# Performance work log

Measured on AMD Instinct MI355X. Metric: run time of the kernel, lower is better.

The kernel has to match this reference:

```python
import jax, jax.numpy as jnp
import numpy as np


def setup_inputs() -> dict:
    key = jax.random.key(0)
    k1, k2 = jax.random.split(key)
    from_points = jax.random.normal(k1, (16384, 64), dtype=jnp.float32)
    to_points = jax.random.normal(k2, (16384, 64), dtype=jnp.float32)
    return {"from_points": from_points, "to_points": to_points}


def reference(from_points, to_points):
    # Squared L2 distance matrix [N, M] via ||a||^2 + ||b||^2 - 2 a.b,
    # avoiding the O(N*M*D) broadcasted intermediate of the original.
    a_sq = jnp.sum(from_points * from_points, axis=-1)          # [N]
    b_sq = jnp.sum(to_points * to_points, axis=-1)              # [M]
    cross = jnp.einsum('nd,md->nm', from_points, to_points)     # [N, M]
    dist_mat = a_sq[:, None] + b_sq[None, :] - 2.0 * cross      # [N, M]
    # Row-wise min (nearest neighbor squared distance), then sum.
    return jnp.sum(jnp.min(dist_mat, axis=1))
```

## Files before the change

kernel.cpp:

```cpp
#include <hip/hip_runtime.h>
#include <stdint.h>

#define N_PTS 16384
#define TSPLITS 32
#define TO_TILES 16
#define FGPB 16
#define NBLOCKS (TSPLITS * (256 / FGPB))

typedef __attribute__((ext_vector_type(4)))  int i32x4;
typedef __attribute__((ext_vector_type(16))) int i32x16;

__device__ __forceinline__ int imin(int a, int b) { return a < b ? a : b; }
__device__ __forceinline__ int itree16(i32x16 a) {
    int m0 = imin(imin(a[0],  a[1]),  a[2]);
    int m1 = imin(imin(a[3],  a[4]),  a[5]);
    int m2 = imin(imin(a[6],  a[7]),  a[8]);
    int m3 = imin(imin(a[9],  a[10]), a[11]);
    int m4 = imin(imin(a[12], a[13]), a[14]);
    int m5 = imin(imin(a[15], m0), m1);
    return imin(imin(imin(m2, m3), m4), m5);
}
__device__ __forceinline__ int q8(float x) {
    int q = __float2int_rn(x);
    return q < -127 ? -127 : (q > 127 ? 127 : q);
}

__global__ __launch_bounds__(256) void prep_kernel(
        const float* __restrict__ from_pts, const float* __restrict__ to_pts,
        float* __restrict__ a_sq, int* __restrict__ bsqi,
        char* __restrict__ BfQ, char* __restrict__ AtoQ,
        float* __restrict__ out) {
    int gid = blockIdx.x * 256 + threadIdx.x;
    int row = gid >> 3;
    int sub = gid & 7;
    bool isFrom = row < N_PTS;
    int r = row & (N_PTS - 1);
    const float* src = isFrom ? from_pts : to_pts;
    float4 v0 = ((const float4*)src)[r * 16 + sub * 2];
    float4 v1 = ((const float4*)src)[r * 16 + sub * 2 + 1];
    float s = v0.x*v0.x + v0.y*v0.y + v0.z*v0.z + v0.w*v0.w
            + v1.x*v1.x + v1.y*v1.y + v1.z*v1.z + v1.w*v1.w;
    s += __shfl_xor(s, 1); s += __shfl_xor(s, 2); s += __shfl_xor(s, 4);
    float sc = isFrom ? -16.0f : 16.0f;
    int q0 = q8(v0.x*sc), q1 = q8(v0.y*sc), q2 = q8(v0.z*sc), q3 = q8(v0.w*sc);
    int q4 = q8(v1.x*sc), q5 = q8(v1.y*sc), q6 = q8(v1.z*sc), q7 = q8(v1.w*sc);
    int2 w;
    w.x = (q0 & 255) | ((q1 & 255) << 8) | ((q2 & 255) << 16) | (q3 << 24);
    w.y = (q4 & 255) | ((q5 & 255) << 8) | ((q6 & 255) << 16) | (q7 << 24);
    int st = r >> 5;
    int m  = r & 31;
    int kb = sub >> 2, h = (sub >> 1) & 1, half8 = sub & 1;
    size_t off = (((size_t)st * 2 + kb) * 64 + h * 32 + m) * 16 + 8 * half8;
    if (isFrom) {
        *(int2*)(BfQ + off) = w;
        if (sub == 0) a_sq[r] = s;
    } else {
        *(int2*)(AtoQ + off) = w;
        if (sub == 0)
            bsqi[st * 32 + ((m >> 2) & 1) * 16 + (m & 3) + 4 * (m >> 3)] =
                __float2int_rn(128.0f * s);
    }
    if (gid == 0) out[0] = 0.0f;
}

__global__ __launch_bounds__(512, 4) void main_kernel(
        const char* __restrict__ BfQ, const char* __restrict__ AtoQ,
        const int* __restrict__ bsqi, int* __restrict__ pmin) {
    __shared__ __align__(16) char abuf[32768];

    const int tid = threadIdx.x;
    const int lane = tid & 63;
    const int l31 = lane & 31;
    const int h   = lane >> 5;
    const int wv  = tid >> 6;
    const int ts  = blockIdx.x >> 4;
    const int bg  = blockIdx.x & 15;
    const int gtb = ts * TO_TILES;

    #pragma unroll
    for (int j2 = 0; j2 < 4; j2++) {
        int j = wv * 4 + j2;
        const char* g = AtoQ +
            (((size_t)(gtb + (j >> 1)) * 2 + (j & 1)) * 64 + lane) * 16;
        char* l = &abuf[j * 1024];
        __builtin_amdgcn_global_load_lds(
            (const __attribute__((address_space(1))) unsigned int*)g,
            (__attribute__((address_space(3))) unsigned int*)l, 16, 0, 0);
    }
    __syncthreads();

    #pragma unroll 1
    for (int f2 = 0; f2 < 2; f2++) {
        const int fg = bg * FGPB + f2 * 8 + wv;
        i32x4 Bf0[2], Bf1[2];
        #pragma unroll
        for (int kb = 0; kb < 2; kb++) {
            Bf0[kb] = *(const i32x4*)(BfQ + (((size_t)(2 * fg)     * 2 + kb) * 64 + lane) * 16);
            Bf1[kb] = *(const i32x4*)(BfQ + (((size_t)(2 * fg + 1) * 2 + kb) * 64 + lane) * 16);
        }
        int rmin0 = 0x7FFFFFFF, rmin1 = 0x7FFFFFFF;

        #pragma unroll 1
        for (int t = 0; t < TO_TILES; t++) {
            i32x4 A0 = *(const i32x4*)&abuf[((t * 2 + 0) * 64 + lane) * 16];
            i32x4 A1 = *(const i32x4*)&abuf[((t * 2 + 1) * 64 + lane) * 16];
            union { int4 f[4]; i32x16 v; } cu;
            const int4* cp = (const int4*)(bsqi + (gtb + t) * 32 + h * 16);
            cu.f[0] = cp[0]; cu.f[1] = cp[1]; cu.f[2] = cp[2]; cu.f[3] = cp[3];

            i32x16 acc0 = __builtin_amdgcn_mfma_i32_32x32x32_i8(A0, Bf0[0], cu.v, 0, 0, 0);
            i32x16 acc1 = __builtin_amdgcn_mfma_i32_32x32x32_i8(A0, Bf1[0], cu.v, 0, 0, 0);
            acc0 = __builtin_amdgcn_mfma_i32_32x32x32_i8(A1, Bf0[1], acc0, 0, 0, 0);
            acc1 = __builtin_amdgcn_mfma_i32_32x32x32_i8(A1, Bf1[1], acc1, 0, 0, 0);
            rmin0 = imin(rmin0, itree16(acc0));
            rmin1 = imin(rmin1, itree16(acc1));
        }

        rmin0 = imin(rmin0, __shfl_xor(rmin0, 32));
        rmin1 = imin(rmin1, __shfl_xor(rmin1, 32));
        if (lane < 32) {
            pmin[(size_t)ts * N_PTS + fg * 64 + l31]      = rmin0;
            pmin[(size_t)ts * N_PTS + fg * 64 + 32 + l31] = rmin1;
        }
    }
}

__global__ __launch_bounds__(256) void finish_kernel(
        const float* __restrict__ a_sq, const int* __restrict__ pmin,
        float* __restrict__ out) {
    int r = blockIdx.x * 256 + threadIdx.x;
    int m = pmin[r];
    #pragma unroll
    for (int s = 1; s < TSPLITS; s++)
        m = imin(m, pmin[(size_t)s * N_PTS + r]);
    float v = a_sq[r] + (float)m * 0.0078125f;
    #pragma unroll
    for (int k = 1; k < 64; k <<= 1) v += __shfl_xor(v, k);
    __shared__ float red[4];
    if ((threadIdx.x & 63) == 0) red[threadIdx.x >> 6] = v;
    __syncthreads();
    if (threadIdx.x == 0)
        atomicAdd(out, red[0] + red[1] + red[2] + red[3]);
}

extern "C" void kernel_launch(void* const* d_in, const int* in_sizes, int n_in,
                              void* d_out, int out_size, void* d_ws, size_t ws_size,
                              hipStream_t stream) {
    const float* from_pts = (const float*)d_in[0];
    const float* to_pts   = (const float*)d_in[1];
    char* ws = (char*)d_ws;
    float* a_sq = (float*)ws;
    int*   bsqi = (int*)(ws + (64 << 10));
    int*   pmin = (int*)(ws + (128 << 10));
    char*  BfQ  = ws + (128 << 10) + (2 << 20);
    char*  AtoQ = ws + (128 << 10) + (3 << 20);

    prep_kernel<<<(2 * N_PTS * 8) / 256, 256, 0, stream>>>(
        from_pts, to_pts, a_sq, bsqi, BfQ, AtoQ, (float*)d_out);
    main_kernel<<<NBLOCKS, 512, 0, stream>>>(BfQ, AtoQ, bsqi, pmin);
    finish_kernel<<<N_PTS / 256, 256, 0, stream>>>(a_sq, pmin, (float*)d_out);
}
```

Before: 83.42 us.

## Switch int8 distance MFMA from 32x32x32 to 16x16x64 with 8 from-tiles per wave

Replaces the 32x32x32 int8 MFMA tiles with 16x16x64 tiles, which cover the full K=64 in one instruction. The quantized data layout in the prep kernel and the b_sq bias layout are reorganized to match. Each wave now keeps eight from-point tiles in registers and loops over 32 to-tiles from LDS, using 256-thread blocks instead of 512. The aim is to cut per-result min-reduction work (4 accumulator values instead of 16) and chained MFMA dependencies, and to raise reuse of each LDS A load across 8 MFMAs. The cost is higher register pressure from B[8] and rmin[8], plus a different occupancy and grid shape.

```diff
diff --git a/kernel.cpp b/kernel.cpp
--- a/kernel.cpp
+++ b/kernel.cpp
@@ -3,23 +3,12 @@
 
 #define N_PTS 16384
 #define TSPLITS 32
-#define TO_TILES 16
-#define FGPB 16
-#define NBLOCKS (TSPLITS * (256 / FGPB))
+#define ATILES 32
+#define NBLOCKS (TSPLITS * 32)
 
-typedef __attribute__((ext_vector_type(4)))  int i32x4;
-typedef __attribute__((ext_vector_type(16))) int i32x16;
+typedef __attribute__((ext_vector_type(4))) int i32x4;
 
 __device__ __forceinline__ int imin(int a, int b) { return a < b ? a : b; }
-__device__ __forceinline__ int itree16(i32x16 a) {
-    int m0 = imin(imin(a[0],  a[1]),  a[2]);
-    int m1 = imin(imin(a[3],  a[4]),  a[5]);
-    int m2 = imin(imin(a[6],  a[7]),  a[8]);
-    int m3 = imin(imin(a[9],  a[10]), a[11]);
-    int m4 = imin(imin(a[12], a[13]), a[14]);
-    int m5 = imin(imin(a[15], m0), m1);
-    return imin(imin(imin(m2, m3), m4), m5);
-}
 __device__ __forceinline__ int q8(float x) {
     int q = __float2int_rn(x);
     return q < -127 ? -127 : (q > 127 ? 127 : q);
@@ -47,41 +36,36 @@
     int2 w;
     w.x = (q0 & 255) | ((q1 & 255) << 8) | ((q2 & 255) << 16) | (q3 << 24);
     w.y = (q4 & 255) | ((q5 & 255) << 8) | ((q6 & 255) << 16) | (q7 << 24);
-    int st = r >> 5;
-    int m  = r & 31;
-    int kb = sub >> 2, h = (sub >> 1) & 1, half8 = sub & 1;
-    size_t off = (((size_t)st * 2 + kb) * 64 + h * 32 + m) * 16 + 8 * half8;
+    int st = r >> 4;
+    int m  = r & 15;
+    int qg = sub >> 1, halfj = sub & 1;
+    size_t off = (((size_t)st * 64) + qg * 16 + m) * 16 + 8 * halfj;
     if (isFrom) {
         *(int2*)(BfQ + off) = w;
         if (sub == 0) a_sq[r] = s;
     } else {
         *(int2*)(AtoQ + off) = w;
-        if (sub == 0)
-            bsqi[st * 32 + ((m >> 2) & 1) * 16 + (m & 3) + 4 * (m >> 3)] =
-                __float2int_rn(128.0f * s);
+        if (sub == 0) bsqi[r] = __float2int_rn(128.0f * s);
     }
     if (gid == 0) out[0] = 0.0f;
 }
 
-__global__ __launch_bounds__(512, 4) void main_kernel(
+__global__ __launch_bounds__(256, 5) void main_kernel(
         const char* __restrict__ BfQ, const char* __restrict__ AtoQ,
         const int* __restrict__ bsqi, int* __restrict__ pmin) {
     __shared__ __align__(16) char abuf[32768];
 
     const int tid = threadIdx.x;
     const int lane = tid & 63;
-    const int l31 = lane & 31;
-    const int h   = lane >> 5;
     const int wv  = tid >> 6;
-    const int ts  = blockIdx.x >> 4;
-    const int bg  = blockIdx.x & 15;
-    const int gtb = ts * TO_TILES;
+    const int ts  = blockIdx.x >> 5;
+    const int bg  = blockIdx.x & 31;
+    const int gst = ts * ATILES;
 
     #pragma unroll
-    for (int j2 = 0; j2 < 4; j2++) {
-        int j = wv * 4 + j2;
-        const char* g = AtoQ +
-            (((size_t)(gtb + (j >> 1)) * 2 + (j & 1)) * 64 + lane) * 16;
+    for (int j2 = 0; j2 < 8; j2++) {
+        int j = wv * 8 + j2;
+        const char* g = AtoQ + ((size_t)(gst + j) * 64 + lane) * 16;
         char* l = &abuf[j * 1024];
         __builtin_amdgcn_global_load_lds(
             (const __attribute__((address_space(1))) unsigned int*)g,
@@ -89,39 +73,39 @@
     }
     __syncthreads();
 
-    #pragma unroll 1
-    for (int f2 = 0; f2 < 2; f2++) {
-        const int fg = bg * FGPB + f2 * 8 + wv;
-        i32x4 Bf0[2], Bf1[2];
+    const int sgb = bg * 32 + wv * 8;
+    i32x4 B[8];
+    #pragma unroll
+    for (int j = 0; j < 8; j++)
+        B[j] = *(const i32x4*)(BfQ + ((size_t)(sgb + j) * 64 + lane) * 16);
+
+    int rmin[8];
+    #pragma unroll
+    for (int j = 0; j < 8; j++) rmin[j] = 0x7FFFFFFF;
+
+    const int qg4 = (lane >> 4) * 4;
+
+    #pragma unroll 2
+    for (int t = 0; t < ATILES; t++) {
+        i32x4 A = *(const i32x4*)&abuf[t * 1024 + lane * 16];
+        i32x4 cu = *(const i32x4*)(bsqi + (gst + t) * 16 + qg4);
         #pragma unroll
-        for (int kb = 0; kb < 2; kb++) {
-            Bf0[kb] = *(const i32x4*)(BfQ + (((size_t)(2 * fg)     * 2 + kb) * 64 + lane) * 16);
-            Bf1[kb] = *(const i32x4*)(BfQ + (((size_t)(2 * fg + 1) * 2 + kb) * 64 + lane) * 16);
+        for (int j = 0; j < 8; j++) {
+            i32x4 acc = __builtin_amdgcn_mfma_i32_16x16x64_i8(A, B[j], cu, 0, 0, 0);
+            rmin[j] = imin(rmin[j],
+                           imin(imin(acc[0], acc[1]), imin(acc[2], acc[3])));
         }
-        int rmin0 = 0x7FFFFFFF, rmin1 = 0x7FFFFFFF;
+    }
 
-        #pragma unroll 1
-        for (int t = 0; t < TO_TILES; t++) {
-            i32x4 A0 = *(const i32x4*)&abuf[((t * 2 + 0) * 64 + lane) * 16];
-            i32x4 A1 = *(const i32x4*)&abuf[((t * 2 + 1) * 64 + lane) * 16];
-            union { int4 f[4]; i32x16 v; } cu;
-            const int4* cp = (const int4*)(bsqi + (gtb + t) * 32 + h * 16);
-            cu.f[0] = cp[0]; cu.f[1] = cp[1]; cu.f[2] = cp[2]; cu.f[3] = cp[3];
-
-            i32x16 acc0 = __builtin_amdgcn_mfma_i32_32x32x32_i8(A0, Bf0[0], cu.v, 0, 0, 0);
-            i32x16 acc1 = __builtin_amdgcn_mfma_i32_32x32x32_i8(A0, Bf1[0], cu.v, 0, 0, 0);
-            acc0 = __builtin_amdgcn_mfma_i32_32x32x32_i8(A1, Bf0[1], acc0, 0, 0, 0);
-            acc1 = __builtin_amdgcn_mfma_i32_32x32x32_i8(A1, Bf1[1], acc1, 0, 0, 0);
-            rmin0 = imin(rmin0, itree16(acc0));
-            rmin1 = imin(rmin1, itree16(acc1));
-        }
-
-        rmin0 = imin(rmin0, __shfl_xor(rmin0, 32));
-        rmin1 = imin(rmin1, __shfl_xor(rmin1, 32));
-        if (lane < 32) {
-            pmin[(size_t)ts * N_PTS + fg * 64 + l31]      = rmin0;
-            pmin[(size_t)ts * N_PTS + fg * 64 + 32 + l31] = rmin1;
-        }
+    #pragma unroll
+    for (int j = 0; j < 8; j++) {
+        rmin[j] = imin(rmin[j], __shfl_xor(rmin[j], 16));
+        rmin[j] = imin(rmin[j], __shfl_xor(rmin[j], 32));
+    }
+    if (lane < 16) {
+        #pragma unroll
+        for (int j = 0; j < 8; j++)
+            pmin[(size_t)ts * N_PTS + (sgb + j) * 16 + lane] = rmin[j];
     }
 }
 
@@ -157,6 +141,6 @@
 
     prep_kernel<<<(2 * N_PTS * 8) / 256, 256, 0, stream>>>(
         from_pts, to_pts, a_sq, bsqi, BfQ, AtoQ, (float*)d_out);
-    main_kernel<<<NBLOCKS, 512, 0, stream>>>(BfQ, AtoQ, bsqi, pmin);
+    main_kernel<<<NBLOCKS, 256, 0, stream>>>(BfQ, AtoQ, bsqi, pmin);
     finish_kernel<<<N_PTS / 256, 256, 0, stream>>>(a_sq, pmin, (float*)d_out);
 }
```

After: 80.65 us. -3.3%, faster.
